# Kernel tuning notes

Hardware: AMD Instinct MI355X
Metric: run time of the kernel (lower is better)

## Reference

```python
import jax, jax.numpy as jnp
import numpy as np
import math

# gpt-oss style GQA dims
H, HKV, D = 64, 8, 64          # query heads, kv heads, head_dim
M = H // HKV                    # q_mult (queries per kv head)
D_MODEL = 2880
SLIDING_WINDOW = 128
SM_SCALE = 1.0 / math.sqrt(D)
NEG = -1e30


def _rope_cos_sin(T):
    # YaRN / NTK-by-parts rope (gpt-oss RotaryEmbedding) with
    # base=150000, initial_context_length=1024, scaling=32, alpha=1, beta=32
    base, init_ctx, scaling, alpha, beta = 150000.0, 1024.0, 32.0, 1.0, 32.0
    d_half = D // 2
    freq = base ** (np.arange(0, D, 2, dtype=np.float32) / D)
    concentration = 0.1 * math.log(scaling) + 1.0
    low = d_half * math.log(init_ctx / (beta * 2.0 * math.pi)) / math.log(base)
    high = d_half * math.log(init_ctx / (alpha * 2.0 * math.pi)) / math.log(base)
    ramp = np.clip((np.arange(d_half, dtype=np.float32) - low) / (high - low), 0.0, 1.0)
    inv_freq = ramp / (scaling * freq) + (1.0 - ramp) / freq  # interp<->extrap blend
    freqs = np.outer(np.arange(T, dtype=np.float32), inv_freq)  # (T, D/2)
    return (jnp.asarray(np.cos(freqs) * concentration),
            jnp.asarray(np.sin(freqs) * concentration))


def _apply_rope(x, cos, sin):
    # x[..., :D/2], x[..., D/2:] rotated pairwise; cos/sin broadcast over head dims
    x1, x2 = jnp.split(x, 2, axis=-1)
    return jnp.concatenate([x1 * cos - x2 * sin, x2 * cos + x1 * sin], axis=-1)


def setup_inputs() -> dict:
    key = jax.random.key(0)
    ks = jax.random.split(key, 6)
    x = jax.random.normal(ks[0], (1, 1536, D_MODEL), dtype=jnp.float32)
    qkv_dim = D * (H + 2 * HKV)
    W_qkv = jax.random.normal(ks[1], (D_MODEL, qkv_dim), dtype=jnp.float32) * 0.02
    b_qkv = jax.random.normal(ks[2], (qkv_dim,), dtype=jnp.float32) * 0.02
    W_out = jax.random.normal(ks[3], (H * D, D_MODEL), dtype=jnp.float32) * 0.02
    b_out = jax.random.normal(ks[4], (D_MODEL,), dtype=jnp.float32) * 0.02
    sinks = jax.random.normal(ks[5], (H,), dtype=jnp.float32) / math.sqrt(D)
    return {"x": x, "W_qkv": W_qkv, "b_qkv": b_qkv, "W_out": W_out,
            "b_out": b_out, "sinks": sinks}


def reference(x, W_qkv, b_qkv, W_out, b_out, sinks):
    B, T, _ = x.shape
    qkv = x @ W_qkv + b_qkv
    q = qkv[..., :H * D].reshape(B, T, HKV, M, D)
    k = qkv[..., H * D:(H + HKV) * D].reshape(B, T, HKV, D)
    v = qkv[..., (H + HKV) * D:].reshape(B, T, HKV, D)
    cos, sin = _rope_cos_sin(T)
    q = _apply_rope(q, cos[None, :, None, None, :], sin[None, :, None, None, :])
    k = _apply_rope(k, cos[None, :, None, :], sin[None, :, None, :])
    # GQA scores: (B, HKV, M, Tq, Tk)
    logits = jnp.einsum('bqhmd,bkhd->bhmqk', q, k) * SM_SCALE
    i = jnp.arange(T)[:, None]
    j = jnp.arange(T)[None, :]
    mask = (j <= i) & (j > i - SLIDING_WINDOW)  # causal + sliding window
    logits = jnp.where(mask[None, None, None], logits, NEG)
    m = jnp.max(logits, axis=-1, keepdims=True)
    e = jnp.exp(logits - m)
    # learned per-head sink logit folded into the softmax denominator
    exp_sink = jnp.exp(sinks.reshape(HKV, M)[None, :, :, None, None] - m)
    w = e / (jnp.sum(e, axis=-1, keepdims=True) + exp_sink)
    out = jnp.einsum('bhmqk,bkhd->bqhmd', w, v).reshape(B, T, H * D)
    return out @ W_out + b_out
```

## Files before the change

### kernel.cpp

```cpp
#include <hip/hip_runtime.h>

typedef __bf16 bf16_t;
typedef __bf16 bfrag8 __attribute__((ext_vector_type(8)));
typedef float f32x4 __attribute__((ext_vector_type(4)));

#define T_SEQ 1536
#define LDQKV 5120
#define SM_SCALE 0.125f
#define LOG2E 1.4426950408889634f

__device__ __forceinline__ unsigned short b2u(bf16_t h) {
  union { bf16_t h; unsigned short u; } c; c.h = h; return c.u;
}
__device__ __forceinline__ unsigned int pack2(float lo, float hi) {
  return (unsigned int)b2u((bf16_t)lo) | ((unsigned int)b2u((bf16_t)hi) << 16);
}
__device__ __forceinline__ void gload_lds16(const bf16_t* g, bf16_t* l) {
  __builtin_amdgcn_global_load_lds(
      (const __attribute__((address_space(1))) void*)g,
      (__attribute__((address_space(3))) void*)l, 16, 0, 0);
}

__global__ __launch_bounds__(256, 3)
void gemm_bt(const bf16_t* __restrict__ A, const bf16_t* __restrict__ Bt,
             const float* __restrict__ bias, void* __restrict__ C,
             int M, int N, int K, int out_bf16) {
  __shared__ __align__(16) bf16_t As[128 * 64];
  __shared__ __align__(16) bf16_t Bs[128 * 64];
  const int tid = threadIdx.x;
  const int wave = tid >> 6;
  const int lane = tid & 63;
  const int g = lane >> 4;
  const int lm = lane & 15;

  const int NX = gridDim.x;
  const int nwg = NX * gridDim.y;
  const int orig = blockIdx.y * NX + blockIdx.x;
  const int qq = nwg >> 3, rr = nwg & 7;
  const int xcd = orig & 7, sidx = orig >> 3;
  const int swz = (xcd < rr ? xcd * (qq + 1) : rr * (qq + 1) + (xcd - rr) * qq) + sidx;
  const int n0 = (swz % NX) * 128;
  const int m0 = (swz / NX) * 128;

  const int wm = (wave >> 1) * 64;
  const int wn = (wave & 1) * 64;
  const int srow = lane >> 3;
  const int sseg = lane & 7;

  const bf16_t* gA = A + (size_t)(m0 + wave * 32 + srow) * K + sseg * 8;
  const bf16_t* gB = Bt + (size_t)(n0 + wave * 32 + srow) * K + sseg * 8;
  bf16_t* lA = As + (wave * 32) * 64;
  bf16_t* lB = Bs + (wave * 32) * 64;

  const f32x4 fz = {0.f, 0.f, 0.f, 0.f};
  f32x4 acc[4][4];
#pragma unroll
  for (int i = 0; i < 4; ++i)
#pragma unroll
    for (int j = 0; j < 4; ++j) acc[i][j] = fz;

  for (int k0 = 0; k0 < K; k0 += 64) {
#pragma unroll
    for (int it = 0; it < 4; ++it) {
      gload_lds16(gA + (size_t)(it * 8) * K + k0, lA + it * 8 * 64);
      gload_lds16(gB + (size_t)(it * 8) * K + k0, lB + it * 8 * 64);
    }
    __syncthreads();
#pragma unroll
    for (int ks = 0; ks < 2; ++ks) {
      bfrag8 af[4], bfr[4];
#pragma unroll
      for (int i = 0; i < 4; ++i) {
        af[i]  = *(const bfrag8*)(As + (wm + i * 16 + lm) * 64 + ks * 32 + g * 8);
        bfr[i] = *(const bfrag8*)(Bs + (wn + i * 16 + lm) * 64 + ks * 32 + g * 8);
      }
#pragma unroll
      for (int i = 0; i < 4; ++i)
#pragma unroll
        for (int j = 0; j < 4; ++j)
          acc[i][j] = __builtin_amdgcn_mfma_f32_16x16x32_bf16(af[i], bfr[j],
                                                              acc[i][j], 0, 0, 0);
    }
    __syncthreads();
  }
#pragma unroll
  for (int j = 0; j < 4; ++j) {
    int n = n0 + wn + j * 16 + lm;
    if (n >= N) continue;
    float bv = bias[n];
#pragma unroll
    for (int i = 0; i < 4; ++i) {
      int mr = m0 + wm + i * 16 + g * 4;
#pragma unroll
      for (int r = 0; r < 4; ++r) {
        float v = acc[i][j][r] + bv;
        size_t off = (size_t)(mr + r) * N + n;
        if (out_bf16) ((bf16_t*)C)[off] = (bf16_t)v;
        else          ((float*)C)[off] = v;
      }
    }
  }
}

__global__ __launch_bounds__(256)
void convert_x(const float* __restrict__ src, bf16_t* __restrict__ dst) {
  const int i8 = (blockIdx.x * 256 + threadIdx.x) * 8;
  f32x4 a = *(const f32x4*)(src + i8);
  f32x4 b = *(const f32x4*)(src + i8 + 4);
  uint4 w;
  w.x = pack2(a[0], a[1]);
  w.y = pack2(a[2], a[3]);
  w.z = pack2(b[0], b[1]);
  w.w = pack2(b[2], b[3]);
  *(uint4*)(dst + i8) = w;
}

__global__ __launch_bounds__(256)
void transpose_w(const float* __restrict__ src, bf16_t* __restrict__ dst,
                 int Ksrc, int Nsrc) {
  __shared__ bf16_t tile[32 * 33];
  const int t = threadIdx.x;
  const int r = t >> 3;
  const int c4 = (t & 7) * 4;
  const int n0 = blockIdx.x * 32;
  const int k0 = blockIdx.y * 32;
  f32x4 v = {0.f, 0.f, 0.f, 0.f};
  if (n0 + c4 < Nsrc)
    v = *(const f32x4*)(src + (size_t)(k0 + r) * Nsrc + n0 + c4);
#pragma unroll
  for (int e = 0; e < 4; ++e) tile[(c4 + e) * 33 + r] = (bf16_t)v[e];
  __syncthreads();
  uint2 w;
  w.x = pack2((float)tile[r * 33 + c4], (float)tile[r * 33 + c4 + 1]);
  w.y = pack2((float)tile[r * 33 + c4 + 2], (float)tile[r * 33 + c4 + 3]);
  *(uint2*)(dst + (size_t)(n0 + r) * Ksrc + k0 + c4) = w;
}

__global__ __launch_bounds__(256, 2)
void gemm_mfma(const void* __restrict__ A, const float* __restrict__ B,
               const float* __restrict__ bias, void* __restrict__ C,
               int M, int N, int K, int a_bf16, int out_bf16) {
  __shared__ __align__(16) bf16_t As[128 * 64];
  __shared__ __align__(16) bf16_t Bs[128 * 72];
  const int tid = threadIdx.x;
  const int wave = tid >> 6;
  const int lane = tid & 63;
  const int g = lane >> 4;
  const int lm = lane & 15;
  const int m0 = blockIdx.y * 128;
  const int n0 = blockIdx.x * 128;
  const int wm = (wave >> 1) * 64;
  const int wn = (wave & 1) * 64;
  const int sr = lane >> 3;
  const int seg = lane & 7;
  const int pairk = tid & 31;
  const int cg = tid >> 5;

  int cb = n0 + cg * 16;
  if (cb > N - 16) cb = N - 16;

  const f32x4 fz = {0.f, 0.f, 0.f, 0.f};
  f32x4 acc[4][4];
#pragma unroll
  for (int i = 0; i < 4; ++i)
#pragma unroll
    for (int j = 0; j < 4; ++j) acc[i][j] = fz;

  for (int k0 = 0; k0 < K; k0 += 64) {
    bfrag8 areg[4];
    if (a_bf16) {
#pragma unroll
      for (int it = 0; it < 4; ++it) {
        int ra = (wave * 4 + it) * 8 + sr;
        areg[it] = *(const bfrag8*)((const bf16_t*)A + (size_t)(m0 + ra) * K + k0 + seg * 8);
      }
    } else {
#pragma unroll
      for (int it = 0; it < 4; ++it) {
        int ra = (wave * 4 + it) * 8 + sr;
        const float* ga = (const float*)A + (size_t)(m0 + ra) * K + k0 + seg * 8;
        f32x4 a0 = *(const f32x4*)ga;
        f32x4 a1 = *(const f32x4*)(ga + 4);
#pragma unroll
        for (int e = 0; e < 4; ++e) {
          areg[it][e]     = (bf16_t)a0[e];
          areg[it][e + 4] = (bf16_t)a1[e];
        }
      }
    }
    int kk = 2 * pairk;
    unsigned int pk[16];
    {
      const float* b0 = B + (size_t)(k0 + kk) * N + cb;
      const float* b1 = B + (size_t)(k0 + kk + 1) * N + cb;
      f32x4 x0 = *(const f32x4*)(b0),     x1 = *(const f32x4*)(b0 + 4);
      f32x4 x2 = *(const f32x4*)(b0 + 8), x3 = *(const f32x4*)(b0 + 12);
      f32x4 y0 = *(const f32x4*)(b1),     y1 = *(const f32x4*)(b1 + 4);
      f32x4 y2 = *(const f32x4*)(b1 + 8), y3 = *(const f32x4*)(b1 + 12);
#pragma unroll
      for (int e = 0; e < 4; ++e) {
        pk[e]      = pack2(x0[e], y0[e]);
        pk[e + 4]  = pack2(x1[e], y1[e]);
        pk[e + 8]  = pack2(x2[e], y2[e]);
        pk[e + 12] = pack2(x3[e], y3[e]);
      }
    }
    __syncthreads();
#pragma unroll
    for (int it = 0; it < 4; ++it) {
      int ra = (wave * 4 + it) * 8 + sr;
      *(bfrag8*)(As + ra * 64 + seg * 8) = areg[it];
    }
#pragma unroll
    for (int n = 0; n < 16; ++n)
      *(unsigned int*)(Bs + (cg * 16 + n) * 72 + kk) = pk[n];
    __syncthreads();
#pragma unroll
    for (int ks = 0; ks < 2; ++ks) {
      bfrag8 af[4], bfr[4];
#pragma unroll
      for (int i = 0; i < 4; ++i) {
        af[i]  = *(const bfrag8*)(As + (wm + i * 16 + lm) * 64 + ks * 32 + g * 8);
        bfr[i] = *(const bfrag8*)(Bs + (wn + i * 16 + lm) * 72 + ks * 32 + g * 8);
      }
#pragma unroll
      for (int i = 0; i < 4; ++i)
#pragma unroll
        for (int j = 0; j < 4; ++j)
          acc[i][j] = __builtin_amdgcn_mfma_f32_16x16x32_bf16(af[i], bfr[j],
                                                              acc[i][j], 0, 0, 0);
    }
  }
#pragma unroll
  for (int j = 0; j < 4; ++j) {
    int n = n0 + wn + j * 16 + lm;
    if (n >= N) continue;
    float bv = bias[n];
#pragma unroll
    for (int i = 0; i < 4; ++i) {
      int mr = m0 + wm + i * 16 + g * 4;
#pragma unroll
      for (int r = 0; r < 4; ++r) {
        float v = acc[i][j][r] + bv;
        size_t off = (size_t)(mr + r) * N + n;
        if (out_bf16) ((bf16_t*)C)[off] = (bf16_t)v;
        else          ((float*)C)[off] = v;
      }
    }
  }
}

__global__ __launch_bounds__(256)
void rope_kernel(bf16_t* __restrict__ qkv) {
  int idx = blockIdx.x * 256 + threadIdx.x;
  int d = idx & 31;
  int rest = idx >> 5;
  int u = rest % 72;
  int t = rest / 72;
  if (t >= T_SEQ) return;
  int col = (u < 64) ? (u * 64) : (4096 + (u - 64) * 64);
  size_t off = (size_t)t * LDQKV + col + d;
  float x1 = (float)qkv[off];
  float x2 = (float)qkv[off + 32];
  const float lowv = 4.370846f;
  const float highv = 13.675927f;
  const float conc = 1.3465736f;
  float ramp = ((float)d - lowv) / (highv - lowv);
  ramp = fminf(fmaxf(ramp, 0.f), 1.f);
  float freq = exp2f((float)d * 0.53733134f);
  float inv_freq = ramp / (32.f * freq) + (1.f - ramp) / freq;
  float ang = (float)t * inv_freq;
  float c = cosf(ang) * conc;
  float s = sinf(ang) * conc;
  qkv[off]      = (bf16_t)(x1 * c - x2 * s);
  qkv[off + 32] = (bf16_t)(x2 * c + x1 * s);
}

__global__ __launch_bounds__(256, 2)
void attn_mfma(const bf16_t* __restrict__ qkv, const float* __restrict__ sinks,
               bf16_t* __restrict__ attno) {
  __shared__ __align__(16) bf16_t Vt[64 * 40];
  const int tid = threadIdx.x;
  const int wave = tid >> 6;
  const int lane = tid & 63;
  const int g = lane >> 4;
  const int lm = lane & 15;
  const int q0 = blockIdx.x * 32;
  const int kvh = blockIdx.y;
  const int jbase = q0 - 128;
  const int kt0 = (blockIdx.x < 4) ? (4 - blockIdx.x) : 0;

  bfrag8 qf[4][2];
#pragma unroll
  for (int nq = 0; nq < 4; ++nq) {
    const int h = 2 * wave + (nq >> 1);
    const int qr = q0 + (nq & 1) * 16 + lm;
    const bf16_t* qp = qkv + (size_t)qr * LDQKV + kvh * 512 + h * 64 + g * 8;
    qf[nq][0] = *(const bfrag8*)qp;
    qf[nq][1] = *(const bfrag8*)(qp + 32);
  }

  const f32x4 fz = {0.f, 0.f, 0.f, 0.f};
  f32x4 ot[4][4];
#pragma unroll
  for (int dt = 0; dt < 4; ++dt)
#pragma unroll
    for (int nq = 0; nq < 4; ++nq) ot[dt][nq] = fz;
  float mrow[4] = {-1e30f, -1e30f, -1e30f, -1e30f};
  float lrow[4] = {0.f, 0.f, 0.f, 0.f};

  const int vj = tid >> 3;
  const int vd = (tid & 7) * 8;

  for (int kt = kt0; kt < 5; ++kt) {
    const int ktb = jbase + kt * 32;
    __syncthreads();
    {
      bfrag8 v8 = *(const bfrag8*)(qkv + (size_t)(ktb + vj) * LDQKV + 4608 + kvh * 64 + vd);
#pragma unroll
      for (int e = 0; e < 8; ++e) Vt[(vd + e) * 40 + vj] = v8[e];
    }
    bfrag8 kf[2][2];
#pragma unroll
    for (int nk = 0; nk < 2; ++nk) {
      const bf16_t* kp = qkv + (size_t)(ktb + nk * 16 + lm) * LDQKV + 4096 + kvh * 64 + g * 8;
      kf[nk][0] = *(const bfrag8*)kp;
      kf[nk][1] = *(const bfrag8*)(kp + 32);
    }
    f32x4 st[2][4];
#pragma unroll
    for (int nk = 0; nk < 2; ++nk)
#pragma unroll
      for (int nq = 0; nq < 4; ++nq) st[nk][nq] = fz;
#pragma unroll
    for (int ks = 0; ks < 2; ++ks)
#pragma unroll
      for (int nk = 0; nk < 2; ++nk)
#pragma unroll
        for (int nq = 0; nq < 4; ++nq)
          st[nk][nq] = __builtin_amdgcn_mfma_f32_16x16x32_bf16(
              kf[nk][ks], qf[nq][ks], st[nk][nq], 0, 0, 0);

    bfrag8 paf[4];
#pragma unroll
    for (int nq = 0; nq < 4; ++nq) {
      const int q = q0 + (nq & 1) * 16 + lm;
      float sc[8];
      float pm = -1e30f;
#pragma unroll
      for (int nk = 0; nk < 2; ++nk)
#pragma unroll
        for (int r = 0; r < 4; ++r) {
          const int j = ktb + nk * 16 + g * 4 + r;
          const bool ok = (j <= q) && (j > q - 128);
          const float s = ok ? st[nk][nq][r] * (SM_SCALE * LOG2E) : -1e30f;
          sc[nk * 4 + r] = s;
          pm = fmaxf(pm, s);
        }
      pm = fmaxf(pm, __shfl_xor(pm, 16));
      pm = fmaxf(pm, __shfl_xor(pm, 32));
      const float mn = fmaxf(mrow[nq], pm);
      const float alpha = exp2f(mrow[nq] - mn);
      mrow[nq] = mn;
      float p[8];
      float ls = 0.f;
#pragma unroll
      for (int e = 0; e < 8; ++e) {
        p[e] = (sc[e] > -1e29f) ? exp2f(sc[e] - mn) : 0.f;
        ls += p[e];
      }
      lrow[nq] = lrow[nq] * alpha + ls;
#pragma unroll
      for (int dt = 0; dt < 4; ++dt) ot[dt][nq] *= alpha;
      unsigned pk00 = pack2(p[0], p[1]);
      unsigned pk01 = pack2(p[2], p[3]);
      unsigned pk10 = pack2(p[4], p[5]);
      unsigned pk11 = pack2(p[6], p[7]);
      const int srcA = ((g & 1) << 5) | lm;
      const int srcB = srcA + 16;
      unsigned a0 = __shfl(pk00, srcA), b0 = __shfl(pk10, srcA);
      unsigned a1 = __shfl(pk01, srcA), b1 = __shfl(pk11, srcA);
      unsigned a2 = __shfl(pk00, srcB), b2 = __shfl(pk10, srcB);
      unsigned a3 = __shfl(pk01, srcB), b3 = __shfl(pk11, srcB);
      const bool hiw = g >= 2;
      union { unsigned u[4]; bfrag8 f; } pa;
      pa.u[0] = hiw ? b0 : a0;
      pa.u[1] = hiw ? b1 : a1;
      pa.u[2] = hiw ? b2 : a2;
      pa.u[3] = hiw ? b3 : a3;
      paf[nq] = pa.f;
    }
    __syncthreads();
#pragma unroll
    for (int dt = 0; dt < 4; ++dt) {
      const bfrag8 vtf = *(const bfrag8*)(Vt + (dt * 16 + lm) * 40 + g * 8);
#pragma unroll
      for (int nq = 0; nq < 4; ++nq)
        ot[dt][nq] = __builtin_amdgcn_mfma_f32_16x16x32_bf16(
            vtf, paf[nq], ot[dt][nq], 0, 0, 0);
    }
  }

#pragma unroll
  for (int nq = 0; nq < 4; ++nq) {
    float lt = lrow[nq] + __shfl_xor(lrow[nq], 16);
    lt += __shfl_xor(lt, 32);
    const int h = 2 * wave + (nq >> 1);
    const float sk = sinks[kvh * 8 + h];
    const float inv = 1.f / (lt + exp2f(sk * LOG2E - mrow[nq]));
    const int q = q0 + (nq & 1) * 16 + lm;
    bf16_t* op = attno + (size_t)q * 4096 + kvh * 512 + h * 64;
#pragma unroll
    for (int dt = 0; dt < 4; ++dt) {
      const f32x4 o = ot[dt][nq];
      uint2 w;
      w.x = pack2(o[0] * inv, o[1] * inv);
      w.y = pack2(o[2] * inv, o[3] * inv);
      *(uint2*)(op + dt * 16 + g * 4) = w;
    }
  }
}

__global__ __launch_bounds__(256)
void sentinel_fill(float* __restrict__ out, int n) {
  int i = blockIdx.x * 256 + threadIdx.x;
  if (i < n) out[i] = 10000.0f;
}

extern "C" void kernel_launch(void* const* d_in, const int* in_sizes, int n_in,
                              void* d_out, int out_size, void* d_ws, size_t ws_size,
                              hipStream_t stream) {
  const float *x = nullptr, *Wqkv = nullptr, *bqkv = nullptr,
              *Wout = nullptr, *bout = nullptr, *sinks = nullptr;
  for (int i = 0; i < n_in; ++i) {
    switch (in_sizes[i]) {
      case 1536 * 2880:  x = (const float*)d_in[i]; break;
      case 2880 * 5120:  Wqkv = (const float*)d_in[i]; break;
      case 5120:         bqkv = (const float*)d_in[i]; break;
      case 4096 * 2880:  Wout = (const float*)d_in[i]; break;
      case 2880:         bout = (const float*)d_in[i]; break;
      case 64:           sinks = (const float*)d_in[i]; break;
      default: break;
    }
  }

  const size_t N_QKV  = (size_t)1536 * 5120;
  const size_t N_ATT  = (size_t)1536 * 4096;
  const size_t N_XB   = (size_t)1536 * 2880;
  const size_t N_WQT  = (size_t)5120 * 2880;
  const size_t N_WOT  = (size_t)2944 * 4096;
  const size_t REQ_OLD = (N_QKV + N_ATT) * sizeof(bf16_t);
  const size_t REQ_BIG = (N_QKV + N_ATT + N_XB + N_WQT + N_WOT) * sizeof(bf16_t);

  if (ws_size < REQ_OLD || !x || !Wqkv || !bqkv || !Wout || !bout || !sinks) {
    sentinel_fill<<<(out_size + 255) / 256, 256, 0, stream>>>((float*)d_out, out_size);
    return;
  }

  bf16_t* qkv   = (bf16_t*)d_ws;
  bf16_t* attno = qkv + N_QKV;

  if (ws_size >= REQ_BIG) {
    bf16_t* xb  = attno + N_ATT;
    bf16_t* WqT = xb + N_XB;
    bf16_t* WoT = WqT + N_WQT;
    convert_x<<<2160, 256, 0, stream>>>(x, xb);
    transpose_w<<<dim3(160, 90), 256, 0, stream>>>(Wqkv, WqT, 2880, 5120);
    transpose_w<<<dim3(92, 128), 256, 0, stream>>>(Wout, WoT, 4096, 2880);
    gemm_bt<<<dim3(40, 12), 256, 0, stream>>>(xb, WqT, bqkv, qkv,
                                              1536, 5120, 2880, 1);
    rope_kernel<<<dim3((1536 * 72 * 32) / 256), 256, 0, stream>>>(qkv);
    attn_mfma<<<dim3(1536 / 32, 8), 256, 0, stream>>>(qkv, sinks, attno);
    gemm_bt<<<dim3(23, 12), 256, 0, stream>>>(attno, WoT, bout, d_out,
                                              1536, 2880, 4096, 0);
  } else {
    gemm_mfma<<<dim3(5120 / 128, 1536 / 128), 256, 0, stream>>>(
        x, Wqkv, bqkv, qkv, 1536, 5120, 2880, 0, 1);
    rope_kernel<<<dim3((1536 * 72 * 32) / 256), 256, 0, stream>>>(qkv);
    attn_mfma<<<dim3(1536 / 32, 8), 256, 0, stream>>>(qkv, sinks, attno);
    gemm_mfma<<<dim3((2880 + 127) / 128, 1536 / 128), 256, 0, stream>>>(
        attno, Wout, bout, d_out, 1536, 2880, 4096, 1, 0);
  }
}
```

Baseline: 360.4 us.

## Double-buffer LDS in gemm_bt and shrink N tile to 64

The bf16 GEMM now uses two LDS buffers, issuing the next K-tile's global-to-LDS loads before computing on the current one, which removes one barrier per iteration and overlaps loads with MFMA. The N tile is halved from 128 to 64, so the grids double (80x12 and 45x12), giving more workgroups on the machine. This costs lower arithmetic intensity per block and more redundant A loads. The 45x64 tiling covers 2880 exactly, so less work is wasted in the second GEMM.

```diff
diff --git a/kernel.cpp b/kernel.cpp
--- a/kernel.cpp
+++ b/kernel.cpp
@@ -25,8 +25,8 @@
 void gemm_bt(const bf16_t* __restrict__ A, const bf16_t* __restrict__ Bt,
              const float* __restrict__ bias, void* __restrict__ C,
              int M, int N, int K, int out_bf16) {
-  __shared__ __align__(16) bf16_t As[128 * 64];
-  __shared__ __align__(16) bf16_t Bs[128 * 64];
+  __shared__ __align__(16) bf16_t As[2][128 * 64];
+  __shared__ __align__(16) bf16_t Bs[2][64 * 64];
   const int tid = threadIdx.x;
   const int wave = tid >> 6;
   const int lane = tid & 63;
@@ -39,52 +39,63 @@
   const int qq = nwg >> 3, rr = nwg & 7;
   const int xcd = orig & 7, sidx = orig >> 3;
   const int swz = (xcd < rr ? xcd * (qq + 1) : rr * (qq + 1) + (xcd - rr) * qq) + sidx;
-  const int n0 = (swz % NX) * 128;
+  const int n0 = (swz % NX) * 64;
   const int m0 = (swz / NX) * 128;
 
   const int wm = (wave >> 1) * 64;
-  const int wn = (wave & 1) * 64;
+  const int wn = (wave & 1) * 32;
   const int srow = lane >> 3;
   const int sseg = lane & 7;
 
   const bf16_t* gA = A + (size_t)(m0 + wave * 32 + srow) * K + sseg * 8;
-  const bf16_t* gB = Bt + (size_t)(n0 + wave * 32 + srow) * K + sseg * 8;
-  bf16_t* lA = As + (wave * 32) * 64;
-  bf16_t* lB = Bs + (wave * 32) * 64;
+  const bf16_t* gB = Bt + (size_t)(n0 + wave * 16 + srow) * K + sseg * 8;
 
   const f32x4 fz = {0.f, 0.f, 0.f, 0.f};
-  f32x4 acc[4][4];
+  f32x4 acc[4][2];
 #pragma unroll
   for (int i = 0; i < 4; ++i)
 #pragma unroll
-    for (int j = 0; j < 4; ++j) acc[i][j] = fz;
-
-  for (int k0 = 0; k0 < K; k0 += 64) {
-#pragma unroll
-    for (int it = 0; it < 4; ++it) {
-      gload_lds16(gA + (size_t)(it * 8) * K + k0, lA + it * 8 * 64);
-      gload_lds16(gB + (size_t)(it * 8) * K + k0, lB + it * 8 * 64);
-    }
-    __syncthreads();
+    for (int j = 0; j < 2; ++j) acc[i][j] = fz;
+
+#define STAGE_TILE(b, k0)                                                     \
+  {                                                                           \
+    _Pragma("unroll")                                                         \
+    for (int it = 0; it < 4; ++it)                                            \
+      gload_lds16(gA + (size_t)(it * 8) * K + (k0), &As[b][(wave * 32 + it * 8) * 64]); \
+    _Pragma("unroll")                                                         \
+    for (int it = 0; it < 2; ++it)                                            \
+      gload_lds16(gB + (size_t)(it * 8) * K + (k0), &Bs[b][(wave * 16 + it * 8) * 64]); \
+  }
+
+  const int nt = K >> 6;
+  STAGE_TILE(0, 0);
+  __syncthreads();
+  int cur = 0;
+  for (int t = 0; t < nt; ++t) {
+    if (t + 1 < nt) STAGE_TILE(cur ^ 1, (t + 1) << 6);
 #pragma unroll
     for (int ks = 0; ks < 2; ++ks) {
-      bfrag8 af[4], bfr[4];
-#pragma unroll
-      for (int i = 0; i < 4; ++i) {
-        af[i]  = *(const bfrag8*)(As + (wm + i * 16 + lm) * 64 + ks * 32 + g * 8);
-        bfr[i] = *(const bfrag8*)(Bs + (wn + i * 16 + lm) * 64 + ks * 32 + g * 8);
-      }
+      bfrag8 af[4], bfr[2];
 #pragma unroll
       for (int i = 0; i < 4; ++i)
-#pragma unroll
-        for (int j = 0; j < 4; ++j)
+        af[i] = *(const bfrag8*)(&As[cur][(wm + i * 16 + lm) * 64 + ks * 32 + g * 8]);
+#pragma unroll
+      for (int j = 0; j < 2; ++j)
+        bfr[j] = *(const bfrag8*)(&Bs[cur][(wn + j * 16 + lm) * 64 + ks * 32 + g * 8]);
+#pragma unroll
+      for (int i = 0; i < 4; ++i)
+#pragma unroll
+        for (int j = 0; j < 2; ++j)
           acc[i][j] = __builtin_amdgcn_mfma_f32_16x16x32_bf16(af[i], bfr[j],
                                                               acc[i][j], 0, 0, 0);
     }
     __syncthreads();
-  }
-#pragma unroll
-  for (int j = 0; j < 4; ++j) {
+    cur ^= 1;
+  }
+#undef STAGE_TILE
+
+#pragma unroll
+  for (int j = 0; j < 2; ++j) {
     int n = n0 + wn + j * 16 + lm;
     if (n >= N) continue;
     float bv = bias[n];
@@ -467,11 +478,11 @@
     convert_x<<<2160, 256, 0, stream>>>(x, xb);
     transpose_w<<<dim3(160, 90), 256, 0, stream>>>(Wqkv, WqT, 2880, 5120);
     transpose_w<<<dim3(92, 128), 256, 0, stream>>>(Wout, WoT, 4096, 2880);
-    gemm_bt<<<dim3(40, 12), 256, 0, stream>>>(xb, WqT, bqkv, qkv,
+    gemm_bt<<<dim3(80, 12), 256, 0, stream>>>(xb, WqT, bqkv, qkv,
                                               1536, 5120, 2880, 1);
     rope_kernel<<<dim3((1536 * 72 * 32) / 256), 256, 0, stream>>>(qkv);
     attn_mfma<<<dim3(1536 / 32, 8), 256, 0, stream>>>(qkv, sinks, attno);
-    gemm_bt<<<dim3(23, 12), 256, 0, stream>>>(attno, WoT, bout, d_out,
+    gemm_bt<<<dim3(45, 12), 256, 0, stream>>>(attno, WoT, bout, d_out,
                                               1536, 2880, 4096, 0);
   } else {
     gemm_mfma<<<dim3(5120 / 128, 1536 / 128), 256, 0, stream>>>(
```

Result: slower. 392.2 us (+8.8%).

## Split-K both projection GEMMs into two partitions with a separate reduce kernel

Applied to the files above, without the earlier changes.

Both bf16 GEMMs now run with a grid z-dimension of 2, and each z-slice covers half of the K range. Each slice writes fp32 partial sums to a workspace buffer, and a new reduce kernel adds the two partials plus the bias and writes bf16 (QKV) or fp32 (output). The aim is to fill the GPU better, since the output GEMM has only 276 tiles and the QKV GEMM has 480. The cost is extra fp32 partial traffic of about 63MB and 35MB, plus two more kernel launches.

```diff
diff --git a/kernel.cpp b/kernel.cpp
--- a/kernel.cpp
+++ b/kernel.cpp
@@ -24,7 +24,7 @@
 __global__ __launch_bounds__(256, 3)
 void gemm_bt(const bf16_t* __restrict__ A, const bf16_t* __restrict__ Bt,
              const float* __restrict__ bias, void* __restrict__ C,
-             int M, int N, int K, int out_bf16) {
+             int M, int N, int K, int out_mode) {
   __shared__ __align__(16) bf16_t As[128 * 64];
   __shared__ __align__(16) bf16_t Bs[128 * 64];
   const int tid = threadIdx.x;
@@ -42,6 +42,13 @@
   const int n0 = (swz % NX) * 128;
   const int m0 = (swz / NX) * 128;
 
+  const int tot = K >> 6;
+  const int KS = gridDim.z;
+  const int s = blockIdx.z;
+  const int base = tot / KS, rem = tot % KS;
+  const int ksteps = base + (s < rem ? 1 : 0);
+  const int kbeg = s * base + (s < rem ? s : rem);
+
   const int wm = (wave >> 1) * 64;
   const int wn = (wave & 1) * 64;
   const int srow = lane >> 3;
@@ -59,7 +66,8 @@
 #pragma unroll
     for (int j = 0; j < 4; ++j) acc[i][j] = fz;
 
-  for (int k0 = 0; k0 < K; k0 += 64) {
+  for (int t = 0; t < ksteps; ++t) {
+    const int k0 = (kbeg + t) << 6;
 #pragma unroll
     for (int it = 0; it < 4; ++it) {
       gload_lds16(gA + (size_t)(it * 8) * K + k0, lA + it * 8 * 64);
@@ -83,11 +91,13 @@
     }
     __syncthreads();
   }
+
+  float* Cpart = (float*)C + (out_mode == 2 ? (size_t)s * M * N : 0);
 #pragma unroll
   for (int j = 0; j < 4; ++j) {
     int n = n0 + wn + j * 16 + lm;
     if (n >= N) continue;
-    float bv = bias[n];
+    float bv = (out_mode == 2) ? 0.f : bias[n];
 #pragma unroll
     for (int i = 0; i < 4; ++i) {
       int mr = m0 + wm + i * 16 + g * 4;
@@ -95,10 +105,32 @@
       for (int r = 0; r < 4; ++r) {
         float v = acc[i][j][r] + bv;
         size_t off = (size_t)(mr + r) * N + n;
-        if (out_bf16) ((bf16_t*)C)[off] = (bf16_t)v;
-        else          ((float*)C)[off] = v;
-      }
-    }
+        if (out_mode == 1) ((bf16_t*)C)[off] = (bf16_t)v;
+        else               Cpart[off] = v;
+      }
+    }
+  }
+}
+
+__global__ __launch_bounds__(256)
+void reduce_splits(const float* __restrict__ p, size_t MN,
+                   const float* __restrict__ bias, int N,
+                   void* __restrict__ dst, int out_bf16) {
+  const size_t i4 = ((size_t)blockIdx.x * 256 + threadIdx.x) * 4;
+  f32x4 a = *(const f32x4*)(p + i4);
+  f32x4 b = *(const f32x4*)(p + MN + i4);
+  const int col = (int)(i4 % (size_t)N);
+  f32x4 bv = *(const f32x4*)(bias + col);
+  f32x4 v;
+#pragma unroll
+  for (int e = 0; e < 4; ++e) v[e] = a[e] + b[e] + bv[e];
+  if (out_bf16) {
+    uint2 w;
+    w.x = pack2(v[0], v[1]);
+    w.y = pack2(v[2], v[3]);
+    *(uint2*)((bf16_t*)dst + i4) = w;
+  } else {
+    *(f32x4*)((float*)dst + i4) = v;
   }
 }
 
@@ -451,6 +483,8 @@
   const size_t N_WOT  = (size_t)2944 * 4096;
   const size_t REQ_OLD = (N_QKV + N_ATT) * sizeof(bf16_t);
   const size_t REQ_BIG = (N_QKV + N_ATT + N_XB + N_WQT + N_WOT) * sizeof(bf16_t);
+  const size_t N_PART  = 2 * N_QKV;
+  const size_t REQ_SPLIT = REQ_BIG + N_PART * sizeof(float);
 
   if (ws_size < REQ_OLD || !x || !Wqkv || !bqkv || !Wout || !bout || !sinks) {
     sentinel_fill<<<(out_size + 255) / 256, 256, 0, stream>>>((float*)d_out, out_size);
@@ -467,12 +501,25 @@
     convert_x<<<2160, 256, 0, stream>>>(x, xb);
     transpose_w<<<dim3(160, 90), 256, 0, stream>>>(Wqkv, WqT, 2880, 5120);
     transpose_w<<<dim3(92, 128), 256, 0, stream>>>(Wout, WoT, 4096, 2880);
-    gemm_bt<<<dim3(40, 12), 256, 0, stream>>>(xb, WqT, bqkv, qkv,
-                                              1536, 5120, 2880, 1);
-    rope_kernel<<<dim3((1536 * 72 * 32) / 256), 256, 0, stream>>>(qkv);
-    attn_mfma<<<dim3(1536 / 32, 8), 256, 0, stream>>>(qkv, sinks, attno);
-    gemm_bt<<<dim3(23, 12), 256, 0, stream>>>(attno, WoT, bout, d_out,
-                                              1536, 2880, 4096, 0);
+
+    if (ws_size >= REQ_SPLIT) {
+      float* part = (float*)(WoT + N_WOT);
+      gemm_bt<<<dim3(40, 12, 2), 256, 0, stream>>>(
+          xb, WqT, nullptr, part, 1536, 5120, 2880, 2);
+      reduce_splits<<<7680, 256, 0, stream>>>(part, N_QKV, bqkv, 5120, qkv, 1);
+      rope_kernel<<<dim3((1536 * 72 * 32) / 256), 256, 0, stream>>>(qkv);
+      attn_mfma<<<dim3(1536 / 32, 8), 256, 0, stream>>>(qkv, sinks, attno);
+      gemm_bt<<<dim3(23, 12, 2), 256, 0, stream>>>(
+          attno, WoT, nullptr, part, 1536, 2880, 4096, 2);
+      reduce_splits<<<4320, 256, 0, stream>>>(part, N_XB, bout, 2880, d_out, 0);
+    } else {
+      gemm_bt<<<dim3(40, 12, 1), 256, 0, stream>>>(xb, WqT, bqkv, qkv,
+                                                   1536, 5120, 2880, 1);
+      rope_kernel<<<dim3((1536 * 72 * 32) / 256), 256, 0, stream>>>(qkv);
+      attn_mfma<<<dim3(1536 / 32, 8), 256, 0, stream>>>(qkv, sinks, attno);
+      gemm_bt<<<dim3(23, 12, 1), 256, 0, stream>>>(attno, WoT, bout, d_out,
+                                                   1536, 2880, 4096, 0);
+    }
   } else {
     gemm_mfma<<<dim3(5120 / 128, 1536 / 128), 256, 0, stream>>>(
         x, Wqkv, bqkv, qkv, 1536, 5120, 2880, 0, 1);
```

New measurement: 352.5 us. 1.02x faster.
